# Performance work log

Measured on AMD Instinct MI355X. Metric: run time of the kernel, lower is better.

## Reference

```python
import jax, jax.numpy as jnp
import numpy as np

B, T, I, H, O = 64, 512, 256, 1024, 256

def setup_inputs() -> dict:
    key = jax.random.key(0)
    ks = jax.random.split(key, 7)
    s_ih = 1.0 / np.sqrt(H)
    return {
        "x": jax.random.normal(ks[0], (B, T, I), dtype=jnp.float32),
        "W_ih": jax.random.uniform(ks[1], (H, I), jnp.float32, -s_ih, s_ih),
        "W_hh": jax.random.uniform(ks[2], (H, H), jnp.float32, -s_ih, s_ih),
        "b_ih": jax.random.uniform(ks[3], (H,), jnp.float32, -s_ih, s_ih),
        "b_hh": jax.random.uniform(ks[4], (H,), jnp.float32, -s_ih, s_ih),
        "W_fc": jax.random.uniform(ks[5], (O, H), jnp.float32, -s_ih, s_ih),
        "b_fc": jax.random.uniform(ks[6], (O,), jnp.float32, -s_ih, s_ih),
    }

def reference(x, W_ih, W_hh, b_ih, b_hh, W_fc, b_fc):
    # Precompute input projections for all timesteps: [T, B, H]
    xp = jnp.einsum('bti,hi->tbh', x, W_ih) + b_ih + b_hh
    h0 = jnp.zeros((x.shape[0], W_hh.shape[0]), dtype=x.dtype)

    def step(h, xp_t):
        h = jnp.tanh(xp_t + h @ W_hh.T)
        return h, None

    h_last, _ = jax.lax.scan(step, h0, xp)
    # Linear head on final hidden state: [B, O]
    return h_last @ W_fc.T + b_fc
```

## Files before the change

### kernel.cpp

```cpp
#include <hip/hip_runtime.h>

#define B_ 64
#define T_ 512
#define I_ 256
#define H_ 1024
#define O_ 256

#define NCLUST 4
#define WPC 64
#define MB 16
#define ROWS 16
#define NMF_H 8
#define NMF_X 2
#define KPW_H 256
#define KPW_X 64
#define SENT 0x7FFF7FFFu

typedef _Float16 f16;
typedef _Float16 f16x2 __attribute__((ext_vector_type(2)));
typedef _Float16 f16x4 __attribute__((ext_vector_type(4)));
typedef _Float16 half8 __attribute__((ext_vector_type(8)));
typedef float floatx4 __attribute__((ext_vector_type(4)));
typedef unsigned int uint4v __attribute__((ext_vector_type(4)));

__device__ __forceinline__ uint4v load_uc16(const void* p) {
  uint4v r;
  asm volatile("global_load_dwordx4 %0, %1, off sc0 sc1" : "=v"(r) : "v"(p));
  return r;
}
__device__ __forceinline__ void store_uc4(void* p, unsigned v) {
  asm volatile("global_store_dword %0, %1, off sc0 sc1" :: "v"(p), "v"(v) : "memory");
}
__device__ __forceinline__ void store_uc16(void* p, uint4v v) {
  asm volatile("global_store_dwordx4 %0, %1, off sc0 sc1" :: "v"(p), "v"(v) : "memory");
}
__device__ __forceinline__ unsigned pack_f16x2(float a, float b) {
  f16x2 t; t[0] = (f16)a; t[1] = (f16)b;
  return __builtin_bit_cast(unsigned, t);
}

#if __has_builtin(__builtin_amdgcn_fdot2)
__device__ __forceinline__ float dot2f(f16x2 a, f16x2 b, float c) {
  return __builtin_amdgcn_fdot2(a, b, c, false);
}
#else
__device__ __forceinline__ float dot2f(f16x2 a, f16x2 b, float c) {
  return fmaf((float)a[0], (float)b[0], fmaf((float)a[1], (float)b[1], c));
}
#endif

__device__ __forceinline__ float dot8f(half8 w, half8 v, float acc) {
  acc = dot2f(__builtin_shufflevector(w, w, 0, 1), __builtin_shufflevector(v, v, 0, 1), acc);
  acc = dot2f(__builtin_shufflevector(w, w, 2, 3), __builtin_shufflevector(v, v, 2, 3), acc);
  acc = dot2f(__builtin_shufflevector(w, w, 4, 5), __builtin_shufflevector(v, v, 4, 5), acc);
  acc = dot2f(__builtin_shufflevector(w, w, 6, 7), __builtin_shufflevector(v, v, 6, 7), acc);
  return acc;
}

__global__ void cast_f16(const float* __restrict__ src, f16* __restrict__ dst, int n4) {
  int i = blockIdx.x * blockDim.x + threadIdx.x;
  if (i >= n4) return;
  float4 a = reinterpret_cast<const float4*>(src)[i];
  f16x4 v;
  v[0] = (f16)a.x; v[1] = (f16)a.y; v[2] = (f16)a.z; v[3] = (f16)a.w;
  reinterpret_cast<f16x4*>(dst)[i] = v;
}

__global__ void convert_T8(const float* __restrict__ src, f16* __restrict__ dst,
                           int R, int K) {
  int K8 = K >> 3;
  int total = R * K8;
  int idx = blockIdx.x * blockDim.x + threadIdx.x;
  if (idx >= total) return;
  int r = idx / K8;
  int k8 = idx - r * K8;
  const float4* s = reinterpret_cast<const float4*>(src + (size_t)r * K + (size_t)k8 * 8);
  float4 a = s[0], b = s[1];
  half8 v;
  v[0] = (f16)a.x; v[1] = (f16)a.y; v[2] = (f16)a.z; v[3] = (f16)a.w;
  v[4] = (f16)b.x; v[5] = (f16)b.y; v[6] = (f16)b.z; v[7] = (f16)b.w;
  reinterpret_cast<half8*>(dst)[(size_t)k8 * R + r] = v;
}

__global__ void init_hseq(unsigned* __restrict__ p, long n16) {
  uint4v sv; sv[0] = SENT; sv[1] = SENT; sv[2] = SENT; sv[3] = SENT;
  long i = (long)blockIdx.x * blockDim.x + threadIdx.x;
  const long stride = (long)gridDim.x * blockDim.x;
  for (; i < n16; i += stride) store_uc16(p + 4 * i, sv);
}

__global__ __launch_bounds__(256) void rnn6(
    const f16* __restrict__ whh,
    const f16* __restrict__ wih,
    const f16* __restrict__ xbf,
    const float* __restrict__ bih,
    const float* __restrict__ bhh,
    f16* __restrict__ hseq) {
  const int wg = blockIdx.x;
  const int c = wg & 3;
  const int w = wg >> 2;
  const int tid = threadIdx.x;
  const int wv = tid >> 6;
  const int lane = tid & 63;
  const int lr = lane & 15;
  const int kb = lane >> 4;
  const int n0 = w * ROWS;
  const int b0 = c * MB;

  half8 bfh[NMF_H];
#pragma unroll
  for (int i = 0; i < NMF_H; ++i) {
    const int k = wv * KPW_H + i * 32 + kb * 8;
    bfh[i] = *reinterpret_cast<const half8*>(&whh[(size_t)(n0 + lr) * H_ + k]);
  }
  half8 bfx[NMF_X];
#pragma unroll
  for (int i = 0; i < NMF_X; ++i) {
    const int k = wv * KPW_X + i * 32 + kb * 8;
    bfx[i] = *reinterpret_cast<const half8*>(&wih[(size_t)(n0 + lr) * I_ + k]);
  }

  const int m = ((lane >> 4) << 2) | wv;
  const int nl = lane & 15;
  const float bias = bih[n0 + nl] + bhh[n0 + nl];

  const f16* xrow = xbf + (size_t)(b0 + lr) * T_ * I_ + wv * KPW_X + kb * 8;

  __shared__ floatx4 red[2][4][64];
  const size_t CST = (size_t)NCLUST * MB * H_;
  const size_t coff = (size_t)c * MB * H_;

  for (int s = 1; s <= T_; ++s) {
    const f16* xs = xrow + (size_t)(s - 1) * I_;
    half8 ax0 = *reinterpret_cast<const half8*>(xs);
    half8 ax1 = *reinterpret_cast<const half8*>(xs + 32);

    floatx4 acc0 = {0.f, 0.f, 0.f, 0.f}, acc1 = {0.f, 0.f, 0.f, 0.f};
    acc0 = __builtin_amdgcn_mfma_f32_16x16x32_f16(ax0, bfx[0], acc0, 0, 0, 0);
    acc1 = __builtin_amdgcn_mfma_f32_16x16x32_f16(ax1, bfx[1], acc1, 0, 0, 0);

    if (s > 1) {
      const f16* hr = hseq + (size_t)(s - 2) * CST + coff;
      uint4v af[NMF_H];
      int g = 0;
      for (;;) {
#pragma unroll
        for (int i = 0; i < NMF_H; ++i) {
          const int k = wv * KPW_H + i * 32 + kb * 8;
          af[i] = load_uc16(&hr[(size_t)lr * H_ + k]);
        }
        asm volatile("s_waitcnt vmcnt(0)" ::: "memory");
        unsigned bad = 0u;
#pragma unroll
        for (int i = 0; i < NMF_H; ++i) {
          bad |= (unsigned)(af[i][0] == SENT);
          bad |= (unsigned)(af[i][1] == SENT);
          bad |= (unsigned)(af[i][2] == SENT);
          bad |= (unsigned)(af[i][3] == SENT);
        }
        if (__all(bad == 0u)) break;
        if (++g > (1 << 14)) break;
        __builtin_amdgcn_s_sleep(1);
      }
      __builtin_amdgcn_sched_barrier(0);
#pragma unroll
      for (int i = 0; i < NMF_H; ++i) {
        half8 a = __builtin_bit_cast(half8, af[i]);
        if (i & 1) acc1 = __builtin_amdgcn_mfma_f32_16x16x32_f16(a, bfh[i], acc1, 0, 0, 0);
        else       acc0 = __builtin_amdgcn_mfma_f32_16x16x32_f16(a, bfh[i], acc0, 0, 0, 0);
      }
    }

    const int pr = s & 1;
    red[pr][wv][lane] = acc0 + acc1;
    __syncthreads();

    float v = red[pr][0][lane][wv] + red[pr][1][lane][wv] +
              red[pr][2][lane][wv] + red[pr][3][lane][wv] + bias;
    float hn = tanhf(v);
    float po = __shfl_xor(hn, 1);
    f16* hw = hseq + (size_t)(s - 1) * CST + coff;
    if (!(lane & 1)) {
      store_uc4(&hw[(size_t)m * H_ + n0 + nl], pack_f16x2(hn, po));
    }
  }
}

__global__ __launch_bounds__(256) void fc_head_flat(
    const f16* __restrict__ hlast, const f16* __restrict__ wfcT,
    const float* __restrict__ bfc, float* __restrict__ out) {
  __shared__ f16 hs[H_];
  const int b = blockIdx.x;
  const int o = threadIdx.x;
  reinterpret_cast<f16x4*>(hs)[o] =
      reinterpret_cast<const f16x4*>(hlast + (size_t)b * H_)[o];
  __syncthreads();
  float acc = bfc[o];
  const half8* wp = reinterpret_cast<const half8*>(wfcT) + o;
  const half8* hv = reinterpret_cast<const half8*>(hs);
#pragma unroll 8
  for (int c8 = 0; c8 < H_ / 8; ++c8) acc = dot8f(wp[(size_t)c8 * O_], hv[c8], acc);
  out[(size_t)b * O_ + o] = acc;
}

__global__ __launch_bounds__(1024) void rnn_f16(
    const float* __restrict__ x, const f16* __restrict__ wihT,
    const f16* __restrict__ whhT, const float* __restrict__ bih,
    const float* __restrict__ bhh, const f16* __restrict__ wfcT,
    const float* __restrict__ bfc, float* __restrict__ out) {
  __shared__ f16 hs[H_];
  __shared__ f16 xs[I_];
  const int b = blockIdx.x;
  const int j = threadIdx.x;
  const float bias = bih[j] + bhh[j];
  hs[j] = (f16)0.f;
  const half8* wih_p = reinterpret_cast<const half8*>(wihT) + j;
  const half8* whh_p = reinterpret_cast<const half8*>(whhT) + j;
  const half8* xv = reinterpret_cast<const half8*>(xs);
  const half8* hv = reinterpret_cast<const half8*>(hs);
  const float* xrow = x + (size_t)b * T_ * I_;
  for (int t = 0; t < T_; ++t) {
    if (j < I_) xs[j] = (f16)xrow[t * I_ + j];
    __syncthreads();
    float acc = bias;
#pragma unroll 8
    for (int c = 0; c < I_ / 8; ++c) acc = dot8f(wih_p[c * H_], xv[c], acc);
#pragma unroll 8
    for (int c = 0; c < H_ / 8; ++c) acc = dot8f(whh_p[c * H_], hv[c], acc);
    float hn = tanhf(acc);
    __syncthreads();
    hs[j] = (f16)hn;
  }
  __syncthreads();
  if (j < O_) {
    const half8* wfc_p = reinterpret_cast<const half8*>(wfcT) + j;
    float acc = bfc[j];
#pragma unroll 8
    for (int c = 0; c < H_ / 8; ++c) acc = dot8f(wfc_p[c * O_], hv[c], acc);
    out[(size_t)b * O_ + j] = acc;
  }
}

__global__ __launch_bounds__(1024) void rnn_fp32(
    const float* __restrict__ x,
    const float* __restrict__ Wih, const float* __restrict__ Whh,
    const float* __restrict__ bih, const float* __restrict__ bhh,
    const float* __restrict__ Wfc, const float* __restrict__ bfc,
    float* __restrict__ out) {
  __shared__ float hs[H_];
  __shared__ float xs[I_];
  const int b = blockIdx.x;
  const int j = threadIdx.x;
  const float bias = bih[j] + bhh[j];
  hs[j] = 0.f;
  const float4* wih_r = reinterpret_cast<const float4*>(Wih + (size_t)j * I_);
  const float4* whh_r = reinterpret_cast<const float4*>(Whh + (size_t)j * H_);
  const float4* xv = reinterpret_cast<const float4*>(xs);
  const float4* hv = reinterpret_cast<const float4*>(hs);
  const float* xrow = x + (size_t)b * T_ * I_;
  for (int t = 0; t < T_; ++t) {
    if (j < I_) xs[j] = xrow[t * I_ + j];
    __syncthreads();
    float acc = bias;
#pragma unroll 4
    for (int c = 0; c < I_ / 4; ++c) {
      float4 w = wih_r[c], v = xv[c];
      acc = fmaf(w.x, v.x, acc); acc = fmaf(w.y, v.y, acc);
      acc = fmaf(w.z, v.z, acc); acc = fmaf(w.w, v.w, acc);
    }
#pragma unroll 4
    for (int c = 0; c < H_ / 4; ++c) {
      float4 w = whh_r[c], v = hv[c];
      acc = fmaf(w.x, v.x, acc); acc = fmaf(w.y, v.y, acc);
      acc = fmaf(w.z, v.z, acc); acc = fmaf(w.w, v.w, acc);
    }
    float hn = tanhf(acc);
    __syncthreads();
    hs[j] = hn;
  }
  __syncthreads();
  if (j < O_) {
    float acc = bfc[j];
    const float4* wfc_r = reinterpret_cast<const float4*>(Wfc + (size_t)j * H_);
    for (int c = 0; c < H_ / 4; ++c) {
      float4 w = wfc_r[c], v = hv[c];
      acc = fmaf(w.x, v.x, acc); acc = fmaf(w.y, v.y, acc);
      acc = fmaf(w.z, v.z, acc); acc = fmaf(w.w, v.w, acc);
    }
    out[(size_t)b * O_ + j] = acc;
  }
}

extern "C" void kernel_launch(void* const* d_in, const int* in_sizes, int n_in,
                              void* d_out, int out_size, void* d_ws, size_t ws_size,
                              hipStream_t stream) {
  const float* x   = (const float*)d_in[0];
  const float* Wih = (const float*)d_in[1];
  const float* Whh = (const float*)d_in[2];
  const float* bih = (const float*)d_in[3];
  const float* bhh = (const float*)d_in[4];
  const float* Wfc = (const float*)d_in[5];
  const float* bfc = (const float*)d_in[6];
  float* out = (float*)d_out;

  const size_t n_whh = (size_t)H_ * H_;
  const size_t n_wih = (size_t)H_ * I_;
  const size_t n_wfc = (size_t)O_ * H_;
  const size_t n_x   = (size_t)B_ * T_ * I_;
  const size_t n_hseq = (size_t)T_ * NCLUST * MB * H_;
  const int thr = 256;

  {
    size_t off = 0;
    const size_t o_whh = off; off += n_whh;
    const size_t o_wih = off; off += n_wih;
    const size_t o_wfc = off; off += n_wfc;
    const size_t o_x   = off; off += n_x;
    const size_t o_hs  = off; off += n_hseq;
    const size_t need1 = off * sizeof(f16);

    if (ws_size >= need1) {
      f16* wsf   = (f16*)d_ws;
      f16* whh_h = wsf + o_whh;
      f16* wih_h = wsf + o_wih;
      f16* wfcT  = wsf + o_wfc;
      f16* xbf   = wsf + o_x;
      f16* hseq  = wsf + o_hs;

      const long n16 = (long)(n_hseq * sizeof(f16) / 16);
      init_hseq<<<4096, thr, 0, stream>>>((unsigned*)hseq, n16);
      cast_f16<<<(int)(n_whh / 4 / thr), thr, 0, stream>>>(Whh, whh_h, (int)(n_whh / 4));
      cast_f16<<<(int)(n_wih / 4 / thr), thr, 0, stream>>>(Wih, wih_h, (int)(n_wih / 4));
      cast_f16<<<(int)(n_x / 4 / thr), thr, 0, stream>>>(x, xbf, (int)(n_x / 4));
      convert_T8<<<(int)(n_wfc / 8 / thr), thr, 0, stream>>>(Wfc, wfcT, O_, H_);

      rnn6<<<NCLUST * WPC, thr, 0, stream>>>(whh_h, wih_h, xbf, bih, bhh, hseq);
      const f16* hlast = hseq + (size_t)(T_ - 1) * NCLUST * MB * H_;
      fc_head_flat<<<B_, O_, 0, stream>>>(hlast, wfcT, bfc, out);
      return;
    }
  }

  if (ws_size >= (n_wih + n_whh + n_wfc) * sizeof(f16)) {
    f16* wihT = (f16*)d_ws;
    f16* whhT = wihT + n_wih;
    f16* wfcT = whhT + n_whh;
    convert_T8<<<(int)((n_wih / 8 + thr - 1) / thr), thr, 0, stream>>>(Wih, wihT, H_, I_);
    convert_T8<<<(int)((n_whh / 8 + thr - 1) / thr), thr, 0, stream>>>(Whh, whhT, H_, H_);
    convert_T8<<<(int)((n_wfc / 8 + thr - 1) / thr), thr, 0, stream>>>(Wfc, wfcT, O_, H_);
    rnn_f16<<<B_, 1024, 0, stream>>>(x, wihT, whhT, bih, bhh, wfcT, bfc, out);
  } else {
    rnn_fp32<<<B_, 1024, 0, stream>>>(x, Wih, Whh, bih, bhh, Wfc, bfc, out);
  }
}
```

Before: 1.170 ms.

## Halve persistent workgroups with 32 rows each, L2-first polling and dual-path stores

The recurrent kernel now gives each workgroup 32 hidden rows instead of 16, so 128 active workgroups run instead of 256. The launch keeps 256 blocks and half exit immediately, apparently to spread the active ones across dies or XCDs. The polling loop re-reads only the fragments still holding sentinels and tries L2-cached loads for the first two attempts before falling back to uncached loads. Each h value is stored both through L2 and uncached. This cuts the number of cross-workgroup sync participants but doubles MFMA work per workgroup, and relies on L2 coherence behaviour across XCDs that may not hold.

```diff
diff --git a/kernel.cpp b/kernel.cpp
--- a/kernel.cpp
+++ b/kernel.cpp
@@ -7,13 +7,9 @@
 #define O_ 256
 
 #define NCLUST 4
-#define WPC 64
+#define WPC 32
 #define MB 16
-#define ROWS 16
-#define NMF_H 8
-#define NMF_X 2
-#define KPW_H 256
-#define KPW_X 64
+#define ROWS 32
 #define SENT 0x7FFF7FFFu
 
 typedef _Float16 f16;
@@ -33,6 +29,18 @@
 }
 __device__ __forceinline__ void store_uc16(void* p, uint4v v) {
   asm volatile("global_store_dwordx4 %0, %1, off sc0 sc1" :: "v"(p), "v"(v) : "memory");
+}
+__device__ __forceinline__ uint4v load_l2_16(const void* p) {
+  uint4v r;
+  asm volatile("global_load_dwordx4 %0, %1, off sc0" : "=v"(r) : "v"(p));
+  return r;
+}
+__device__ __forceinline__ void store_l2_4(void* p, unsigned v) {
+  asm volatile("global_store_dword %0, %1, off sc0" :: "v"(p), "v"(v) : "memory");
+}
+__device__ __forceinline__ void store_dual(void* p, unsigned v) {
+  store_l2_4(p, v);
+  store_uc4(p, v);
 }
 __device__ __forceinline__ unsigned pack_f16x2(float a, float b) {
   f16x2 t; t[0] = (f16)a; t[1] = (f16)b;
@@ -89,7 +97,7 @@
   for (; i < n16; i += stride) store_uc16(p + 4 * i, sv);
 }
 
-__global__ __launch_bounds__(256) void rnn6(
+__global__ __launch_bounds__(256) void rnn8(
     const f16* __restrict__ whh,
     const f16* __restrict__ wih,
     const f16* __restrict__ xbf,
@@ -97,8 +105,9 @@
     const float* __restrict__ bhh,
     f16* __restrict__ hseq) {
   const int wg = blockIdx.x;
-  const int c = wg & 3;
-  const int w = wg >> 2;
+  const int c = wg & 7;
+  if (c >= NCLUST) return;
+  const int w = wg >> 3;
   const int tid = threadIdx.x;
   const int wv = tid >> 6;
   const int lane = tid & 63;
@@ -107,26 +116,28 @@
   const int n0 = w * ROWS;
   const int b0 = c * MB;
 
-  half8 bfh[NMF_H];
-#pragma unroll
-  for (int i = 0; i < NMF_H; ++i) {
-    const int k = wv * KPW_H + i * 32 + kb * 8;
-    bfh[i] = *reinterpret_cast<const half8*>(&whh[(size_t)(n0 + lr) * H_ + k]);
-  }
-  half8 bfx[NMF_X];
-#pragma unroll
-  for (int i = 0; i < NMF_X; ++i) {
-    const int k = wv * KPW_X + i * 32 + kb * 8;
-    bfx[i] = *reinterpret_cast<const half8*>(&wih[(size_t)(n0 + lr) * I_ + k]);
+  half8 bfh0[8], bfh1[8], bfx0[2], bfx1[2];
+#pragma unroll
+  for (int i = 0; i < 8; ++i) {
+    const int k = wv * 256 + i * 32 + kb * 8;
+    bfh0[i] = *reinterpret_cast<const half8*>(&whh[(size_t)(n0 + lr) * H_ + k]);
+    bfh1[i] = *reinterpret_cast<const half8*>(&whh[(size_t)(n0 + 16 + lr) * H_ + k]);
+  }
+#pragma unroll
+  for (int j = 0; j < 2; ++j) {
+    const int k = wv * 64 + j * 32 + kb * 8;
+    bfx0[j] = *reinterpret_cast<const half8*>(&wih[(size_t)(n0 + lr) * I_ + k]);
+    bfx1[j] = *reinterpret_cast<const half8*>(&wih[(size_t)(n0 + 16 + lr) * I_ + k]);
   }
 
   const int m = ((lane >> 4) << 2) | wv;
   const int nl = lane & 15;
-  const float bias = bih[n0 + nl] + bhh[n0 + nl];
-
-  const f16* xrow = xbf + (size_t)(b0 + lr) * T_ * I_ + wv * KPW_X + kb * 8;
-
-  __shared__ floatx4 red[2][4][64];
+  const float bias0 = bih[n0 + nl] + bhh[n0 + nl];
+  const float bias1 = bih[n0 + 16 + nl] + bhh[n0 + 16 + nl];
+
+  const f16* xrow = xbf + (size_t)(b0 + lr) * T_ * I_ + wv * 64 + kb * 8;
+
+  __shared__ floatx4 red[2][2][4][64];
   const size_t CST = (size_t)NCLUST * MB * H_;
   const size_t coff = (size_t)c * MB * H_;
 
@@ -135,53 +146,75 @@
     half8 ax0 = *reinterpret_cast<const half8*>(xs);
     half8 ax1 = *reinterpret_cast<const half8*>(xs + 32);
 
-    floatx4 acc0 = {0.f, 0.f, 0.f, 0.f}, acc1 = {0.f, 0.f, 0.f, 0.f};
-    acc0 = __builtin_amdgcn_mfma_f32_16x16x32_f16(ax0, bfx[0], acc0, 0, 0, 0);
-    acc1 = __builtin_amdgcn_mfma_f32_16x16x32_f16(ax1, bfx[1], acc1, 0, 0, 0);
+    floatx4 p0 = {0.f,0.f,0.f,0.f}, p1 = {0.f,0.f,0.f,0.f};
+    floatx4 q0 = {0.f,0.f,0.f,0.f}, q1 = {0.f,0.f,0.f,0.f};
+    p0 = __builtin_amdgcn_mfma_f32_16x16x32_f16(ax0, bfx0[0], p0, 0, 0, 0);
+    p1 = __builtin_amdgcn_mfma_f32_16x16x32_f16(ax1, bfx0[1], p1, 0, 0, 0);
+    q0 = __builtin_amdgcn_mfma_f32_16x16x32_f16(ax0, bfx1[0], q0, 0, 0, 0);
+    q1 = __builtin_amdgcn_mfma_f32_16x16x32_f16(ax1, bfx1[1], q1, 0, 0, 0);
 
     if (s > 1) {
       const f16* hr = hseq + (size_t)(s - 2) * CST + coff;
-      uint4v af[NMF_H];
+      uint4v af[8];
+      unsigned need = 0xFFu;
       int g = 0;
       for (;;) {
 #pragma unroll
-        for (int i = 0; i < NMF_H; ++i) {
-          const int k = wv * KPW_H + i * 32 + kb * 8;
-          af[i] = load_uc16(&hr[(size_t)lr * H_ + k]);
+        for (int i = 0; i < 8; ++i) {
+          if (need & (1u << i)) {
+            const f16* p = &hr[(size_t)lr * H_ + wv * 256 + i * 32 + kb * 8];
+            if (g < 2) af[i] = load_l2_16(p);
+            else       af[i] = load_uc16(p);
+          }
         }
         asm volatile("s_waitcnt vmcnt(0)" ::: "memory");
-        unsigned bad = 0u;
-#pragma unroll
-        for (int i = 0; i < NMF_H; ++i) {
-          bad |= (unsigned)(af[i][0] == SENT);
-          bad |= (unsigned)(af[i][1] == SENT);
-          bad |= (unsigned)(af[i][2] == SENT);
-          bad |= (unsigned)(af[i][3] == SENT);
+        unsigned nn = 0u;
+#pragma unroll
+        for (int i = 0; i < 8; ++i) {
+          if (need & (1u << i)) {
+            unsigned bad = (unsigned)(af[i][0] == SENT) | (unsigned)(af[i][1] == SENT) |
+                           (unsigned)(af[i][2] == SENT) | (unsigned)(af[i][3] == SENT);
+            nn |= bad << i;
+          }
         }
-        if (__all(bad == 0u)) break;
-        if (++g > (1 << 14)) break;
+        need = nn;
+        if (__all(need == 0u)) break;
+        if (++g > (1 << 12)) break;
         __builtin_amdgcn_s_sleep(1);
       }
       __builtin_amdgcn_sched_barrier(0);
 #pragma unroll
-      for (int i = 0; i < NMF_H; ++i) {
+      for (int i = 0; i < 8; ++i) {
         half8 a = __builtin_bit_cast(half8, af[i]);
-        if (i & 1) acc1 = __builtin_amdgcn_mfma_f32_16x16x32_f16(a, bfh[i], acc1, 0, 0, 0);
-        else       acc0 = __builtin_amdgcn_mfma_f32_16x16x32_f16(a, bfh[i], acc0, 0, 0, 0);
+        if (i & 1) {
+          p1 = __builtin_amdgcn_mfma_f32_16x16x32_f16(a, bfh0[i], p1, 0, 0, 0);
+          q1 = __builtin_amdgcn_mfma_f32_16x16x32_f16(a, bfh1[i], q1, 0, 0, 0);
+        } else {
+          p0 = __builtin_amdgcn_mfma_f32_16x16x32_f16(a, bfh0[i], p0, 0, 0, 0);
+          q0 = __builtin_amdgcn_mfma_f32_16x16x32_f16(a, bfh1[i], q0, 0, 0, 0);
+        }
       }
     }
 
     const int pr = s & 1;
-    red[pr][wv][lane] = acc0 + acc1;
-    __syncthreads();
-
-    float v = red[pr][0][lane][wv] + red[pr][1][lane][wv] +
-              red[pr][2][lane][wv] + red[pr][3][lane][wv] + bias;
-    float hn = tanhf(v);
-    float po = __shfl_xor(hn, 1);
+    red[pr][0][wv][lane] = p0 + p1;
+    red[pr][1][wv][lane] = q0 + q1;
+    __syncthreads();
+
     f16* hw = hseq + (size_t)(s - 1) * CST + coff;
-    if (!(lane & 1)) {
-      store_uc4(&hw[(size_t)m * H_ + n0 + nl], pack_f16x2(hn, po));
+    {
+      float v0 = red[pr][0][0][lane][wv] + red[pr][0][1][lane][wv] +
+                 red[pr][0][2][lane][wv] + red[pr][0][3][lane][wv] + bias0;
+      float h0v = tanhf(v0);
+      float po0 = __shfl_xor(h0v, 1);
+      float v1 = red[pr][1][0][lane][wv] + red[pr][1][1][lane][wv] +
+                 red[pr][1][2][lane][wv] + red[pr][1][3][lane][wv] + bias1;
+      float h1v = tanhf(v1);
+      float po1 = __shfl_xor(h1v, 1);
+      if (!(lane & 1)) {
+        store_dual(&hw[(size_t)m * H_ + n0 + nl], pack_f16x2(h0v, po0));
+        store_dual(&hw[(size_t)m * H_ + n0 + 16 + nl], pack_f16x2(h1v, po1));
+      }
     }
   }
 }
@@ -334,7 +367,7 @@
       cast_f16<<<(int)(n_x / 4 / thr), thr, 0, stream>>>(x, xbf, (int)(n_x / 4));
       convert_T8<<<(int)(n_wfc / 8 / thr), thr, 0, stream>>>(Wfc, wfcT, O_, H_);
 
-      rnn6<<<NCLUST * WPC, thr, 0, stream>>>(whh_h, wih_h, xbf, bih, bhh, hseq);
+      rnn8<<<256, thr, 0, stream>>>(whh_h, wih_h, xbf, bih, bhh, hseq);
       const f16* hlast = hseq + (size_t)(T_ - 1) * NCLUST * MB * H_;
       fc_head_flat<<<B_, O_, 0, stream>>>(hlast, wfcT, bfc, out);
       return;
```

Result: slower. 2.677 ms (+128.8%).
